# Performance work log

Hardware: AMD Instinct MI355X
Metric: run time of the kernel (lower is better)

## Reference

```python
import jax, jax.numpy as jnp
import numpy as np

N_HEADS = 16
MAX_CACHE_LEN = 8192
LN_EPS = 1e-5


def _layernorm(x, g, b):
    mu = jnp.mean(x, axis=-1, keepdims=True)
    var = jnp.var(x, axis=-1, keepdims=True)
    return (x - mu) * jax.lax.rsqrt(var + LN_EPS) * g + b


def setup_inputs() -> dict:
    key = jax.random.key(0)
    ks = jax.random.split(key, 8)
    b, t, d, latdim, past = 2, 2048, 2048, 512, 2048
    s = 0.02
    return {
        "x": jax.random.normal(ks[0], (b, t, d), jnp.float32),
        "latent_prev": jax.random.normal(ks[1], (b, past, latdim), jnp.float32),
        "Wq": jax.random.normal(ks[2], (d, d), jnp.float32) * s,
        "Wdown": jax.random.normal(ks[3], (d, latdim), jnp.float32) * s,
        "Wk_up": jax.random.normal(ks[4], (latdim, d), jnp.float32) * s,
        "Wv_up": jax.random.normal(ks[5], (latdim, d), jnp.float32) * s,
        "ln_g": jnp.ones((latdim,), jnp.float32),
        "ln_b": jnp.zeros((latdim,), jnp.float32),
        "Wo": jax.random.normal(ks[6], (d, d), jnp.float32) * s,
    }


def reference(x, latent_prev, Wq, Wdown, Wk_up, Wv_up, ln_g, ln_b, Wo):
    b, t, d = x.shape
    H = N_HEADS
    hd = d // H
    # q projection -> [b, t, H, hd]
    q = (x @ Wq).reshape(b, t, H, hd)
    # latent down-projection + LayerNorm, concat with cache, trim to max_cache_len
    latent_new = _layernorm(x @ Wdown, ln_g, ln_b)
    latent = jnp.concatenate([latent_prev, latent_new], axis=1)
    latent = latent[:, -MAX_CACHE_LEN:]
    S = latent.shape[1]
    past_len = min(latent_prev.shape[1], S - t)
    # up-project K/V from latent -> [b, S, H, hd]
    k = (latent @ Wk_up).reshape(b, S, H, hd)
    v = (latent @ Wv_up).reshape(b, S, H, hd)
    # offset-causal SDPA: query i attends keys j <= past_len + i
    scores = jnp.einsum("bthd,bshd->bhts", q, k) / jnp.sqrt(jnp.asarray(hd, x.dtype))
    i = jnp.arange(t)[:, None]
    j = jnp.arange(S)[None, :]
    mask = j <= (past_len + i)  # [t, S]
    scores = jnp.where(mask[None, None], scores, jnp.asarray(-1e30, scores.dtype))
    attn = jax.nn.softmax(scores, axis=-1)
    out = jnp.einsum("bhts,bshd->bthd", attn, v).reshape(b, t, d)
    return out @ Wo
```

## Files before the change

### kernel.cpp

```cpp
#include <hip/hip_runtime.h>
#include <hip/hip_bf16.h>

using bf16_t = __bf16;
typedef __bf16 bf16x8 __attribute__((ext_vector_type(8)));
typedef __bf16 bf16x4 __attribute__((ext_vector_type(4)));
typedef __bf16 bf16x2 __attribute__((ext_vector_type(2)));
typedef float  f32x4  __attribute__((ext_vector_type(4)));
typedef float  f32x16 __attribute__((ext_vector_type(16)));
typedef unsigned u32x4 __attribute__((ext_vector_type(4)));

#define MFMA16(a,b,c) __builtin_amdgcn_mfma_f32_16x16x32_bf16((a),(b),(c),0,0,0)
#define MFMA32(a,b,c) __builtin_amdgcn_mfma_f32_32x32x16_bf16((a),(b),(c),0,0,0)

__device__ __forceinline__ void load_lds16(const void* g, void* l) {
  __builtin_amdgcn_global_load_lds(
      (const __attribute__((address_space(1))) unsigned int*)g,
      (__attribute__((address_space(3))) unsigned int*)l, 16, 0, 0);
}

__device__ __forceinline__ unsigned pack_bf16(float a, float b) {
  union { bf16x2 v; unsigned u; } c;
  c.v[0] = (bf16_t)a; c.v[1] = (bf16_t)b;
  return c.u;
}

__device__ __forceinline__ float fast_exp2(float x) {
#if __has_builtin(__builtin_amdgcn_exp2f)
  return __builtin_amdgcn_exp2f(x);
#else
  return exp2f(x);
#endif
}

__device__ __forceinline__ void xcd_remap(unsigned& bx, unsigned& by,
                                          unsigned& bz)
{
  const unsigned nxy = gridDim.x * gridDim.y;
  const unsigned nwg = nxy * gridDim.z;
  unsigned wg = (blockIdx.z * gridDim.y + blockIdx.y) * gridDim.x + blockIdx.x;
  if ((nwg & 7u) == 0u)
    wg = (wg & 7u) * (nwg >> 3) + (wg >> 3);
  bz = wg / nxy; wg -= bz * nxy;
  by = wg / gridDim.x;
  bx = wg - by * gridDim.x;
}

__global__ __launch_bounds__(256) void cvt_f2b(const float* __restrict__ in,
                                               bf16_t* __restrict__ out)
{
  const size_t i = ((size_t)blockIdx.x * 256 + threadIdx.x) * 4;
  f32x4 d = *(const f32x4*)(in + i);
  bf16x4 o;
#pragma unroll
  for (int j = 0; j < 4; ++j) o[j] = (bf16_t)d[j];
  *(bf16x4*)(out + i) = o;
}

__global__ __launch_bounds__(256) void cvt_transpose(const float* __restrict__ in,
                                                     bf16_t* __restrict__ out,
                                                     int R, int C)
{
  __shared__ __align__(16) bf16_t t[64 * 80];
  const int r0 = blockIdx.y * 64, c0 = blockIdx.x * 64;
  const int rr = threadIdx.x >> 4;
  const int c4 = (threadIdx.x & 15) * 4;
#pragma unroll
  for (int i = 0; i < 4; ++i) {
    const int r = rr + i * 16;
    f32x4 d = *(const f32x4*)(in + (size_t)(r0 + r) * C + c0 + c4);
#pragma unroll
    for (int j = 0; j < 4; ++j) t[(c4 + j) * 80 + r] = (bf16_t)d[j];
  }
  __syncthreads();
  const int a  = threadIdx.x >> 3;
  const int bc = (threadIdx.x & 7) * 8;
#pragma unroll
  for (int half = 0; half < 2; ++half) {
    const int cc = a + half * 32;
    bf16x8 d = *(const bf16x8*)&t[cc * 80 + bc];
    *(bf16x8*)(out + (size_t)(c0 + cc) * R + r0 + bc) = d;
  }
}

template <typename OutT>
__global__ __launch_bounds__(256) void gemm128(const bf16_t* __restrict__ A,
                                               const bf16_t* __restrict__ BT,
                                               OutT* __restrict__ C,
                                               int M, int N, int K, float scale,
                                               long long zB, long long zC)
{
  __shared__ __align__(16) bf16_t As[128 * 64];
  __shared__ __align__(16) bf16_t Bs[128 * 64];
  const int tid = threadIdx.x;
  unsigned bx, by, bz;
  xcd_remap(bx, by, bz);
  BT += (size_t)bz * zB;
  C  += (size_t)bz * zC;
  const int m0 = by * 128, n0 = bx * 128;
  const int lane = tid & 63, w = tid >> 6;
  const int quad = lane >> 4, l15 = lane & 15;
  const int wm = (w >> 1) * 64, wn = (w & 1) * 64;
  const int s_row = tid >> 3;
  const int g_off = ((tid & 7) ^ (s_row & 7)) * 8;
  const bf16_t* Ap = A  + (size_t)(m0 + s_row) * K + g_off;
  const bf16_t* Bp = BT + (size_t)(n0 + s_row) * K + g_off;
  const int cpos0 = (quad ^ (l15 & 7)) * 8;
  const int cpos1 = ((4 + quad) ^ (l15 & 7)) * 8;

  f32x4 acc[4][4] = {};

  for (int k0 = 0; k0 < K; k0 += 64) {
    __syncthreads();
#pragma unroll
    for (int p = 0; p < 4; ++p) {
      load_lds16(Ap + (size_t)(32 * p) * K + k0, As + (tid + 256 * p) * 8);
      load_lds16(Bp + (size_t)(32 * p) * K + k0, Bs + (tid + 256 * p) * 8);
    }
    __syncthreads();
#pragma unroll
    for (int kk = 0; kk < 2; ++kk) {
      const int cp = kk ? cpos1 : cpos0;
      bf16x8 af[4], bfr[4];
#pragma unroll
      for (int fi = 0; fi < 4; ++fi)
        af[fi] = *(const bf16x8*)&As[(wm + fi * 16 + l15) * 64 + cp];
#pragma unroll
      for (int fj = 0; fj < 4; ++fj)
        bfr[fj] = *(const bf16x8*)&Bs[(wn + fj * 16 + l15) * 64 + cp];
#pragma unroll
      for (int fi = 0; fi < 4; ++fi)
#pragma unroll
        for (int fj = 0; fj < 4; ++fj)
          acc[fi][fj] = MFMA16(af[fi], bfr[fj], acc[fi][fj]);
    }
  }

#pragma unroll
  for (int fi = 0; fi < 4; ++fi)
#pragma unroll
    for (int fj = 0; fj < 4; ++fj)
#pragma unroll
      for (int r = 0; r < 4; ++r) {
        const int row = m0 + wm + fi * 16 + quad * 4 + r;
        const int col = n0 + wn + fj * 16 + l15;
        C[(size_t)row * N + col] = (OutT)(acc[fi][fj][r] * scale);
      }
}

__global__ __launch_bounds__(256) void gemm128_dual(const bf16_t* __restrict__ A,
                                                    const bf16_t* __restrict__ BT,
                                                    bf16_t* __restrict__ C1,
                                                    bf16_t* __restrict__ C2,
                                                    float qscale)
{
  __shared__ __align__(16) bf16_t As[128 * 64];
  __shared__ __align__(16) bf16_t Bs[128 * 64];
  const int tid = threadIdx.x;
  unsigned bx, by, bz;
  xcd_remap(bx, by, bz);
  const int K = 2048;
  const int m0 = by * 128, n0 = bx * 128;
  const int lane = tid & 63, w = tid >> 6;
  const int quad = lane >> 4, l15 = lane & 15;
  const int wm = (w >> 1) * 64, wn = (w & 1) * 64;
  const int s_row = tid >> 3;
  const int g_off = ((tid & 7) ^ (s_row & 7)) * 8;
  const bf16_t* Ap = A  + (size_t)(m0 + s_row) * K + g_off;
  const bf16_t* Bp = BT + (size_t)(n0 + s_row) * K + g_off;
  const int cpos0 = (quad ^ (l15 & 7)) * 8;
  const int cpos1 = ((4 + quad) ^ (l15 & 7)) * 8;

  f32x4 acc[4][4] = {};

  for (int k0 = 0; k0 < K; k0 += 64) {
    __syncthreads();
#pragma unroll
    for (int p = 0; p < 4; ++p) {
      load_lds16(Ap + (size_t)(32 * p) * K + k0, As + (tid + 256 * p) * 8);
      load_lds16(Bp + (size_t)(32 * p) * K + k0, Bs + (tid + 256 * p) * 8);
    }
    __syncthreads();
#pragma unroll
    for (int kk = 0; kk < 2; ++kk) {
      const int cp = kk ? cpos1 : cpos0;
      bf16x8 af[4], bfr[4];
#pragma unroll
      for (int fi = 0; fi < 4; ++fi)
        af[fi] = *(const bf16x8*)&As[(wm + fi * 16 + l15) * 64 + cp];
#pragma unroll
      for (int fj = 0; fj < 4; ++fj)
        bfr[fj] = *(const bf16x8*)&Bs[(wn + fj * 16 + l15) * 64 + cp];
#pragma unroll
      for (int fi = 0; fi < 4; ++fi)
#pragma unroll
        for (int fj = 0; fj < 4; ++fj)
          acc[fi][fj] = MFMA16(af[fi], bfr[fj], acc[fi][fj]);
    }
  }

  const bool isQ = (n0 < 2048);
  const float sc = isQ ? qscale : 1.0f;
#pragma unroll
  for (int fi = 0; fi < 4; ++fi)
#pragma unroll
    for (int fj = 0; fj < 4; ++fj)
#pragma unroll
      for (int r = 0; r < 4; ++r) {
        const int row = m0 + wm + fi * 16 + quad * 4 + r;
        const int col = n0 + wn + fj * 16 + l15;
        if (isQ)
          C1[(size_t)row * 2048 + col] = (bf16_t)(acc[fi][fj][r] * sc);
        else
          C2[(size_t)row * 512 + (col - 2048)] = (bf16_t)(acc[fi][fj][r] * sc);
      }
}

__global__ __launch_bounds__(256) void ln_copy(const bf16_t* __restrict__ in,
                                               const float* __restrict__ g_,
                                               const float* __restrict__ b_,
                                               const float* __restrict__ prev,
                                               bf16_t* __restrict__ latent)
{
  const int tid = threadIdx.x;
  if (blockIdx.x >= 4096) {
    const size_t v    = (size_t)(blockIdx.x - 4096) * 256 + tid;
    const size_t flat = v * 4;
    const size_t per  = (size_t)2048 * 512;
    const size_t b    = flat / per, rem = flat % per;
    f32x4 d = *(const f32x4*)(prev + flat);
    bf16x4 o;
#pragma unroll
    for (int j = 0; j < 4; ++j) o[j] = (bf16_t)d[j];
    *(bf16x4*)(latent + b * ((size_t)4096 * 512) + rem) = o;
    return;
  }
  const int row = blockIdx.x;
  const float x0 = (float)in[(size_t)row * 512 + tid];
  const float x1 = (float)in[(size_t)row * 512 + 256 + tid];
  float s  = x0 + x1;
  float sq = x0 * x0 + x1 * x1;
#pragma unroll
  for (int off = 1; off < 64; off <<= 1) {
    s  += __shfl_xor(s, off);
    sq += __shfl_xor(sq, off);
  }
  __shared__ float red[8];
  const int w = tid >> 6;
  if ((tid & 63) == 0) { red[w] = s; red[4 + w] = sq; }
  __syncthreads();
  s  = red[0] + red[1] + red[2] + red[3];
  sq = red[4] + red[5] + red[6] + red[7];
  const float mu   = s * (1.0f / 512.0f);
  const float var  = sq * (1.0f / 512.0f) - mu * mu;
  const float rstd = rsqrtf(var + 1e-5f);
  const int b = row >> 11, tt = row & 2047;
  bf16_t* outp = latent + ((size_t)b * 4096 + 2048 + tt) * 512;
  outp[tid]       = (bf16_t)((x0 - mu) * rstd * g_[tid]       + b_[tid]);
  outp[tid + 256] = (bf16_t)((x1 - mu) * rstd * g_[tid + 256] + b_[tid + 256]);
}

__global__ __launch_bounds__(256) void attn7(const bf16_t* __restrict__ q,
                                             const bf16_t* __restrict__ k,
                                             const bf16_t* __restrict__ vT,
                                             bf16_t* __restrict__ out)
{
  __shared__ __align__(16) bf16_t smem[32768];

  const int tid = threadIdx.x;
  const int lane = tid & 63, w = tid >> 6;
  const int l31 = lane & 31, h5 = lane >> 5;

  const int g = blockIdx.x & 7, j = blockIdx.x >> 3;
  const int jl = j & 31, hsel = j >> 5;
  int qt = jl & 15;
  const int b = jl >> 4;
  if (hsel) qt = 15 - qt;
  const int h = g + 8 * hsel;

  const int q0 = qt * 128;
  const int qg = q0 + l31 * 4 + w;

  bf16x8 qf[8];
  const bf16_t* qb = q + ((size_t)(b * 2048 + qg)) * 2048 + h * 128 + h5 * 8;
#pragma unroll
  for (int fc = 0; fc < 8; ++fc) qf[fc] = *(const bf16x8*)(qb + fc * 16);

  const bf16_t* kbase = k + ((size_t)b * 4096) * 2048 + h * 128;
  const bf16_t* vbase = vT + ((size_t)(b * 16 + h)) * 128 * 4096;

  int ks_key[4], ks_go[4], vs_feat[4], vs_go[4];
#pragma unroll
  for (int p = 0; p < 4; ++p) {
    const int slot = tid + 256 * p;
    const int key = slot >> 4, ph = slot & 15;
    ks_key[p] = key;
    ks_go[p]  = (((ph & 8) | ((ph & 7) ^ (key & 7)))) * 8;
    const int ft = slot >> 3, p2 = slot & 7;
    vs_feat[p] = ft;
    vs_go[p]   = (p2 ^ (ft & 7)) * 8;
  }
  int kfo[8], vfo[4];
#pragma unroll
  for (int fc = 0; fc < 8; ++fc) {
    const int L = fc * 2 + h5;
    kfo[fc] = l31 * 128 + ((L & 8) | ((L & 7) ^ (l31 & 7))) * 8;
  }
#pragma unroll
  for (int kc = 0; kc < 4; ++kc) {
    const int L = kc * 2 + h5;
    vfo[kc] = l31 * 64 + (L ^ (l31 & 7)) * 8;
  }

  f32x16 o[4] = {};
  float m = -1e30f, l = 0.f;
  const int send = 2048 + q0 + 128;

#pragma unroll
  for (int p = 0; p < 4; ++p) {
    load_lds16(kbase + (size_t)ks_key[p] * 2048 + ks_go[p],
               smem + (tid + 256 * p) * 8);
    load_lds16(vbase + (size_t)vs_feat[p] * 4096 + vs_go[p],
               smem + 16384 + (tid + 256 * p) * 8);
  }
  __syncthreads();

  int cur = 0;
  for (int s0 = 0; s0 < send; s0 += 64) {
    const int s1 = s0 + 64;
    if (s1 < send) {
      const int nxt = (cur ^ 1) * 8192;
#pragma unroll
      for (int p = 0; p < 4; ++p) {
        load_lds16(kbase + (size_t)(s1 + ks_key[p]) * 2048 + ks_go[p],
                   smem + nxt + (tid + 256 * p) * 8);
        load_lds16(vbase + (size_t)vs_feat[p] * 4096 + s1 + vs_go[p],
                   smem + 16384 + nxt + (tid + 256 * p) * 8);
      }
    }
    const bf16_t* Kc = smem + cur * 8192;
    const bf16_t* Vc = smem + 16384 + cur * 8192;

    f32x16 st[2] = {};
    __builtin_amdgcn_s_setprio(1);
#pragma unroll
    for (int fc = 0; fc < 8; ++fc) {
      bf16x8 k0 = *(const bf16x8*)&Kc[kfo[fc]];
      bf16x8 k1 = *(const bf16x8*)&Kc[4096 + kfo[fc]];
      st[0] = MFMA32(k0, qf[fc], st[0]);
      st[1] = MFMA32(k1, qf[fc], st[1]);
    }
    __builtin_amdgcn_s_setprio(0);

    if (s0 + 63 > 2048 + q0) {
#pragma unroll
      for (int t = 0; t < 2; ++t)
#pragma unroll
        for (int i = 0; i < 16; ++i) {
          const int key = s0 + 32 * t + (i & 3) + 8 * (i >> 2) + 4 * h5;
          if (key > 2048 + qg) st[t][i] = -1e30f;
        }
    }

    float gm[8];
#pragma unroll
    for (int t = 0; t < 2; ++t)
#pragma unroll
      for (int gg = 0; gg < 4; ++gg)
        gm[t * 4 + gg] = fmaxf(fmaxf(st[t][4 * gg + 0], st[t][4 * gg + 1]),
                               fmaxf(st[t][4 * gg + 2], st[t][4 * gg + 3]));
    float mt = fmaxf(fmaxf(fmaxf(gm[0], gm[1]), fmaxf(gm[2], gm[3])),
                     fmaxf(fmaxf(gm[4], gm[5]), fmaxf(gm[6], gm[7])));
    mt = fmaxf(mt, __shfl_xor(mt, 32));

    if (__any(mt > m + 8.f)) {
      const float mnew = fmaxf(m, mt);
      const float alpha = fast_exp2(m - mnew);
#pragma unroll
      for (int ft = 0; ft < 4; ++ft)
#pragma unroll
        for (int i = 0; i < 16; ++i) o[ft][i] *= alpha;
      l *= alpha;
      m = mnew;
    }

    float rs = 0.f;
    unsigned up[2][4][2];
#pragma unroll
    for (int t = 0; t < 2; ++t)
#pragma unroll
      for (int gg = 0; gg < 4; ++gg) {
        const float p0 = fast_exp2(st[t][4 * gg + 0] - m);
        const float p1 = fast_exp2(st[t][4 * gg + 1] - m);
        const float p2 = fast_exp2(st[t][4 * gg + 2] - m);
        const float p3 = fast_exp2(st[t][4 * gg + 3] - m);
        rs += (p0 + p1) + (p2 + p3);
        up[t][gg][0] = pack_bf16(p0, p1);
        up[t][gg][1] = pack_bf16(p2, p3);
      }
    rs += __shfl_xor(rs, 32);
    l += rs;

#pragma unroll
    for (int kc = 0; kc < 4; ++kc) {
      const int t = kc >> 1, gp = (kc & 1) * 2;
      const unsigned a0 = up[t][gp][0],     a1 = up[t][gp][1];
      const unsigned b0 = up[t][gp + 1][0], b1 = up[t][gp + 1][1];
      const unsigned xa0 = __shfl_xor(a0, 32), xa1 = __shfl_xor(a1, 32);
      const unsigned xb0 = __shfl_xor(b0, 32), xb1 = __shfl_xor(b1, 32);
      u32x4 uw;
      uw[0] = h5 ? xb0 : a0;
      uw[1] = h5 ? xb1 : a1;
      uw[2] = h5 ? b0 : xa0;
      uw[3] = h5 ? b1 : xa1;
      union { u32x4 u; bf16x8 v; } pc; pc.u = uw;
      const bf16x8 pf = pc.v;
      __builtin_amdgcn_s_setprio(1);
#pragma unroll
      for (int ft = 0; ft < 4; ++ft) {
        bf16x8 vf = *(const bf16x8*)&Vc[ft * 2048 + vfo[kc]];
        o[ft] = MFMA32(vf, pf, o[ft]);
      }
      __builtin_amdgcn_s_setprio(0);
    }

    __syncthreads();
    cur ^= 1;
  }

  const float inv = 1.0f / l;
  const int rowp_w = w * 32 + l31;
#pragma unroll
  for (int ft = 0; ft < 4; ++ft)
#pragma unroll
    for (int gg = 0; gg < 4; ++gg) {
      bf16x4 pk;
#pragma unroll
      for (int r = 0; r < 4; ++r) pk[r] = (bf16_t)(o[ft][4 * gg + r] * inv);
      *(bf16x4*)&smem[rowp_w * 136 + ft * 32 + gg * 8 + h5 * 4] = pk;
    }
  __syncthreads();
#pragma unroll
  for (int p = 0; p < 8; ++p) {
    const int c = tid + 256 * p;
    const int rowp = c >> 4, chk = c & 15;
    const int ql = (rowp & 31) * 4 + (rowp >> 5);
    bf16x8 d = *(const bf16x8*)&smem[rowp * 136 + chk * 8];
    *(bf16x8*)(out + ((size_t)(b * 2048 + q0 + ql)) * 2048 + h * 128 + chk * 8) = d;
  }
}

extern "C" void kernel_launch(void* const* d_in, const int* in_sizes, int n_in,
                              void* d_out, int out_size, void* d_ws, size_t ws_size,
                              hipStream_t stream)
{
  (void)in_sizes; (void)n_in; (void)out_size; (void)ws_size;
  const float* x        = (const float*)d_in[0];
  const float* lat_prev = (const float*)d_in[1];
  const float* Wq       = (const float*)d_in[2];
  const float* Wdown    = (const float*)d_in[3];
  const float* Wk_up    = (const float*)d_in[4];
  const float* Wv_up    = (const float*)d_in[5];
  const float* ln_g     = (const float*)d_in[6];
  const float* ln_b     = (const float*)d_in[7];
  const float* Wo       = (const float*)d_in[8];
  float* out = (float*)d_out;

  char* p = (char*)d_ws;
  auto alloc = [&](size_t elems) { bf16_t* r = (bf16_t*)p; p += elems * 2; return r; };
  bf16_t* xb     = alloc((size_t)4096 * 2048);
  bf16_t* WqT    = alloc((size_t)2048 * 2048);
  bf16_t* WdT    = alloc((size_t)512 * 2048);
  bf16_t* qbuf   = alloc((size_t)4096 * 2048);
  bf16_t* latpre = alloc((size_t)4096 * 512);
  bf16_t* latent = alloc((size_t)2 * 4096 * 512);
  bf16_t* kbuf   = alloc((size_t)8192 * 2048);
  bf16_t* vTb    = alloc((size_t)2 * 2048 * 4096);
  bf16_t* aout   = alloc((size_t)4096 * 2048);
  bf16_t* WoT  = xb;
  bf16_t* WkT  = latpre;
  bf16_t* WvT  = latpre + (size_t)2048 * 512;

  const dim3 B(256);
  const float qscale = 0.12751744561825988f;

  cvt_f2b<<<dim3(8192), B, 0, stream>>>(x, xb);
  cvt_transpose<<<dim3(32, 32), B, 0, stream>>>(Wq,    WqT, 2048, 2048);
  cvt_transpose<<<dim3(8,  32), B, 0, stream>>>(Wdown, WdT, 2048, 512);
  gemm128_dual<<<dim3(20, 32), B, 0, stream>>>(xb, WqT, qbuf, latpre, qscale);
  ln_copy<<<dim3(6144), B, 0, stream>>>(latpre, ln_g, ln_b, lat_prev, latent);
  cvt_transpose<<<dim3(32, 32), B, 0, stream>>>(Wo,    WoT, 2048, 2048);
  cvt_transpose<<<dim3(32, 8),  B, 0, stream>>>(Wk_up, WkT, 512, 2048);
  cvt_transpose<<<dim3(32, 8),  B, 0, stream>>>(Wv_up, WvT, 512, 2048);
  gemm128<bf16_t><<<dim3(16, 64), B, 0, stream>>>(latent, WkT, kbuf, 8192, 2048, 512, 1.0f, 0, 0);
  gemm128<bf16_t><<<dim3(32, 16, 2), B, 0, stream>>>(WvT, latent, vTb, 2048, 4096, 512, 1.0f,
                                                     (long long)4096 * 512,
                                                     (long long)2048 * 4096);
  attn7<<<dim3(512), B, 0, stream>>>(qbuf, kbuf, vTb, aout);
  gemm128<float><<<dim3(16, 32), B, 0, stream>>>(aout, WoT, out, 4096, 2048, 2048, 1.0f, 0, 0);
}
```

Measured before the change: 530.5 us.

## Merge prep conversions into one launch and fuse K/V up-projection GEMMs

All fp32-to-bf16 conversions and weight transposes, including the latent cache copy, now run in a single prep_all launch with block-range dispatch. The K and V up-projection GEMMs are fused into one gemm_kv launch with an XCD-aware block remap, and LayerNorm gets its own kernel. The aim is to cut the number of kernel launches and the tail idle time between small kernels. In exchange, WoT, WkT and WvT get dedicated workspace buffers instead of aliasing xb and latpre, which uses more memory.

```diff
diff --git a/kernel.cpp b/kernel.cpp
--- a/kernel.cpp
+++ b/kernel.cpp
@@ -45,25 +45,14 @@
   bx = wg - by * gridDim.x;
 }
 
-__global__ __launch_bounds__(256) void cvt_f2b(const float* __restrict__ in,
-                                               bf16_t* __restrict__ out)
-{
-  const size_t i = ((size_t)blockIdx.x * 256 + threadIdx.x) * 4;
-  f32x4 d = *(const f32x4*)(in + i);
-  bf16x4 o;
-#pragma unroll
-  for (int j = 0; j < 4; ++j) o[j] = (bf16_t)d[j];
-  *(bf16x4*)(out + i) = o;
-}
-
-__global__ __launch_bounds__(256) void cvt_transpose(const float* __restrict__ in,
-                                                     bf16_t* __restrict__ out,
-                                                     int R, int C)
-{
-  __shared__ __align__(16) bf16_t t[64 * 80];
-  const int r0 = blockIdx.y * 64, c0 = blockIdx.x * 64;
-  const int rr = threadIdx.x >> 4;
-  const int c4 = (threadIdx.x & 15) * 4;
+__device__ __forceinline__ void transpose_body(const float* __restrict__ in,
+                                               bf16_t* __restrict__ out,
+                                               int R, int C, int bx, int by,
+                                               int tid, bf16_t* t)
+{
+  const int r0 = by * 64, c0 = bx * 64;
+  const int rr = tid >> 4;
+  const int c4 = (tid & 15) * 4;
 #pragma unroll
   for (int i = 0; i < 4; ++i) {
     const int r = rr + i * 16;
@@ -72,13 +61,60 @@
     for (int j = 0; j < 4; ++j) t[(c4 + j) * 80 + r] = (bf16_t)d[j];
   }
   __syncthreads();
-  const int a  = threadIdx.x >> 3;
-  const int bc = (threadIdx.x & 7) * 8;
+  const int a  = tid >> 3;
+  const int bc = (tid & 7) * 8;
 #pragma unroll
   for (int half = 0; half < 2; ++half) {
     const int cc = a + half * 32;
     bf16x8 d = *(const bf16x8*)&t[cc * 80 + bc];
     *(bf16x8*)(out + (size_t)(c0 + cc) * R + r0 + bc) = d;
+  }
+}
+
+__global__ __launch_bounds__(256) void prep_all(
+    const float* __restrict__ x,     bf16_t* __restrict__ xb,
+    const float* __restrict__ Wq,    bf16_t* __restrict__ WqT,
+    const float* __restrict__ Wdown, bf16_t* __restrict__ WdT,
+    const float* __restrict__ Wo,    bf16_t* __restrict__ WoT,
+    const float* __restrict__ Wk,    bf16_t* __restrict__ WkT,
+    const float* __restrict__ Wv,    bf16_t* __restrict__ WvT,
+    const float* __restrict__ prev,  bf16_t* __restrict__ latent)
+{
+  __shared__ __align__(16) bf16_t t[64 * 80];
+  const int tid = threadIdx.x;
+  const unsigned bid = blockIdx.x;
+  if (bid < 8192) {
+    const size_t i = ((size_t)bid * 256 + tid) * 4;
+    f32x4 d = *(const f32x4*)(x + i);
+    bf16x4 o;
+#pragma unroll
+    for (int j = 0; j < 4; ++j) o[j] = (bf16_t)d[j];
+    *(bf16x4*)(xb + i) = o;
+  } else if (bid < 9216) {
+    const unsigned u = bid - 8192;
+    transpose_body(Wq, WqT, 2048, 2048, u & 31, u >> 5, tid, t);
+  } else if (bid < 9472) {
+    const unsigned u = bid - 9216;
+    transpose_body(Wdown, WdT, 2048, 512, u & 7, u >> 3, tid, t);
+  } else if (bid < 10496) {
+    const unsigned u = bid - 9472;
+    transpose_body(Wo, WoT, 2048, 2048, u & 31, u >> 5, tid, t);
+  } else if (bid < 10752) {
+    const unsigned u = bid - 10496;
+    transpose_body(Wk, WkT, 512, 2048, u & 31, u >> 5, tid, t);
+  } else if (bid < 11008) {
+    const unsigned u = bid - 10752;
+    transpose_body(Wv, WvT, 512, 2048, u & 31, u >> 5, tid, t);
+  } else {
+    const size_t v    = (size_t)(bid - 11008) * 256 + tid;
+    const size_t flat = v * 4;
+    const size_t per  = (size_t)2048 * 512;
+    const size_t b    = flat / per, rem = flat % per;
+    f32x4 d = *(const f32x4*)(prev + flat);
+    bf16x4 o;
+#pragma unroll
+    for (int j = 0; j < 4; ++j) o[j] = (bf16_t)d[j];
+    *(bf16x4*)(latent + b * ((size_t)4096 * 512) + rem) = o;
   }
 }
 
@@ -215,26 +251,92 @@
       }
 }
 
-__global__ __launch_bounds__(256) void ln_copy(const bf16_t* __restrict__ in,
-                                               const float* __restrict__ g_,
-                                               const float* __restrict__ b_,
-                                               const float* __restrict__ prev,
-                                               bf16_t* __restrict__ latent)
-{
+__global__ __launch_bounds__(256) void gemm_kv(const bf16_t* __restrict__ latent,
+                                               const bf16_t* __restrict__ WkT,
+                                               const bf16_t* __restrict__ WvT,
+                                               bf16_t* __restrict__ kbuf,
+                                               bf16_t* __restrict__ vTb)
+{
+  __shared__ __align__(16) bf16_t As[128 * 64];
+  __shared__ __align__(16) bf16_t Bs[128 * 64];
   const int tid = threadIdx.x;
-  if (blockIdx.x >= 4096) {
-    const size_t v    = (size_t)(blockIdx.x - 4096) * 256 + tid;
-    const size_t flat = v * 4;
-    const size_t per  = (size_t)2048 * 512;
-    const size_t b    = flat / per, rem = flat % per;
-    f32x4 d = *(const f32x4*)(prev + flat);
-    bf16x4 o;
-#pragma unroll
-    for (int j = 0; j < 4; ++j) o[j] = (bf16_t)d[j];
-    *(bf16x4*)(latent + b * ((size_t)4096 * 512) + rem) = o;
-    return;
-  }
+  unsigned wg = blockIdx.x;
+  wg = (wg & 7u) * 256u + (wg >> 3);
+  const bf16_t *A, *BT;
+  bf16_t* C;
+  int M, N;
+  unsigned bx, by;
+  if (wg < 1024) {
+    bx = wg & 15; by = wg >> 4;
+    A = latent; BT = WkT; C = kbuf; M = 8192; N = 2048;
+  } else {
+    const unsigned t2 = wg - 1024;
+    const unsigned bz = t2 >> 9, rem = t2 & 511;
+    bx = rem & 31; by = rem >> 5;
+    A  = WvT;
+    BT = latent + (size_t)bz * ((size_t)4096 * 512);
+    C  = vTb + (size_t)bz * ((size_t)2048 * 4096);
+    M = 2048; N = 4096;
+  }
+  const int K = 512;
+  const int m0 = by * 128, n0 = bx * 128;
+  const int lane = tid & 63, w = tid >> 6;
+  const int quad = lane >> 4, l15 = lane & 15;
+  const int wm = (w >> 1) * 64, wn = (w & 1) * 64;
+  const int s_row = tid >> 3;
+  const int g_off = ((tid & 7) ^ (s_row & 7)) * 8;
+  const bf16_t* Ap = A  + (size_t)(m0 + s_row) * K + g_off;
+  const bf16_t* Bp = BT + (size_t)(n0 + s_row) * K + g_off;
+  const int cpos0 = (quad ^ (l15 & 7)) * 8;
+  const int cpos1 = ((4 + quad) ^ (l15 & 7)) * 8;
+
+  f32x4 acc[4][4] = {};
+
+  for (int k0 = 0; k0 < K; k0 += 64) {
+    __syncthreads();
+#pragma unroll
+    for (int p = 0; p < 4; ++p) {
+      load_lds16(Ap + (size_t)(32 * p) * K + k0, As + (tid + 256 * p) * 8);
+      load_lds16(Bp + (size_t)(32 * p) * K + k0, Bs + (tid + 256 * p) * 8);
+    }
+    __syncthreads();
+#pragma unroll
+    for (int kk = 0; kk < 2; ++kk) {
+      const int cp = kk ? cpos1 : cpos0;
+      bf16x8 af[4], bfr[4];
+#pragma unroll
+      for (int fi = 0; fi < 4; ++fi)
+        af[fi] = *(const bf16x8*)&As[(wm + fi * 16 + l15) * 64 + cp];
+#pragma unroll
+      for (int fj = 0; fj < 4; ++fj)
+        bfr[fj] = *(const bf16x8*)&Bs[(wn + fj * 16 + l15) * 64 + cp];
+#pragma unroll
+      for (int fi = 0; fi < 4; ++fi)
+#pragma unroll
+        for (int fj = 0; fj < 4; ++fj)
+          acc[fi][fj] = MFMA16(af[fi], bfr[fj], acc[fi][fj]);
+    }
+  }
+
+#pragma unroll
+  for (int fi = 0; fi < 4; ++fi)
+#pragma unroll
+    for (int fj = 0; fj < 4; ++fj)
+#pragma unroll
+      for (int r = 0; r < 4; ++r) {
+        const int row = m0 + wm + fi * 16 + quad * 4 + r;
+        const int col = n0 + wn + fj * 16 + l15;
+        C[(size_t)row * N + col] = (bf16_t)acc[fi][fj][r];
+      }
+}
+
+__global__ __launch_bounds__(256) void ln_kernel(const bf16_t* __restrict__ in,
+                                                 const float* __restrict__ g_,
+                                                 const float* __restrict__ b_,
+                                                 bf16_t* __restrict__ latent)
+{
   const int row = blockIdx.x;
+  const int tid = threadIdx.x;
   const float x0 = (float)in[(size_t)row * 512 + tid];
   const float x1 = (float)in[(size_t)row * 512 + 256 + tid];
   float s  = x0 + x1;
@@ -476,25 +578,19 @@
   bf16_t* kbuf   = alloc((size_t)8192 * 2048);
   bf16_t* vTb    = alloc((size_t)2 * 2048 * 4096);
   bf16_t* aout   = alloc((size_t)4096 * 2048);
-  bf16_t* WoT  = xb;
-  bf16_t* WkT  = latpre;
-  bf16_t* WvT  = latpre + (size_t)2048 * 512;
+  bf16_t* WoT    = alloc((size_t)2048 * 2048);
+  bf16_t* WkT    = alloc((size_t)2048 * 512);
+  bf16_t* WvT    = alloc((size_t)2048 * 512);
 
   const dim3 B(256);
   const float qscale = 0.12751744561825988f;
 
-  cvt_f2b<<<dim3(8192), B, 0, stream>>>(x, xb);
-  cvt_transpose<<<dim3(32, 32), B, 0, stream>>>(Wq,    WqT, 2048, 2048);
-  cvt_transpose<<<dim3(8,  32), B, 0, stream>>>(Wdown, WdT, 2048, 512);
+  prep_all<<<dim3(13056), B, 0, stream>>>(x, xb, Wq, WqT, Wdown, WdT,
+                                          Wo, WoT, Wk_up, WkT, Wv_up, WvT,
+                                          lat_prev, latent);
   gemm128_dual<<<dim3(20, 32), B, 0, stream>>>(xb, WqT, qbuf, latpre, qscale);
-  ln_copy<<<dim3(6144), B, 0, stream>>>(latpre, ln_g, ln_b, lat_prev, latent);
-  cvt_transpose<<<dim3(32, 32), B, 0, stream>>>(Wo,    WoT, 2048, 2048);
-  cvt_transpose<<<dim3(32, 8),  B, 0, stream>>>(Wk_up, WkT, 512, 2048);
-  cvt_transpose<<<dim3(32, 8),  B, 0, stream>>>(Wv_up, WvT, 512, 2048);
-  gemm128<bf16_t><<<dim3(16, 64), B, 0, stream>>>(latent, WkT, kbuf, 8192, 2048, 512, 1.0f, 0, 0);
-  gemm128<bf16_t><<<dim3(32, 16, 2), B, 0, stream>>>(WvT, latent, vTb, 2048, 4096, 512, 1.0f,
-                                                     (long long)4096 * 512,
-                                                     (long long)2048 * 4096);
+  ln_kernel<<<dim3(4096), B, 0, stream>>>(latpre, ln_g, ln_b, latent);
+  gemm_kv<<<dim3(2048), B, 0, stream>>>(latent, WkT, WvT, kbuf, vTb);
   attn7<<<dim3(512), B, 0, stream>>>(qbuf, kbuf, vTb, aout);
   gemm128<float><<<dim3(16, 32), B, 0, stream>>>(aout, WoT, out, 4096, 2048, 2048, 1.0f, 0, 0);
 }
```

New measurement: 506.8 us. -4.5%, faster.
